# Kernel optimization log

Hardware: AMD Instinct MI355X
Metric: run time of the kernel (lower is better)

The kernel has to match this reference:

```python
import jax, jax.numpy as jnp
import numpy as np

B, T, C = 2, 4096, 1024
H = 16            # n_head (== n_groups == n_kv_heads)
HD = C // H       # head_dim = 64
W = 256           # window_size
ROPE_BASE = 10000.0


def _rope(x):
    # x: (B, H, T, HD); rotate interleaved pairs with position along axis 2
    t = x.shape[2]
    inv_freq = 1.0 / (ROPE_BASE ** (jnp.arange(0, HD, 2, dtype=jnp.float32) / HD))  # (HD/2,)
    freqs = jnp.arange(t, dtype=jnp.float32)[:, None] * inv_freq[None, :]           # (T, HD/2)
    cos = jnp.cos(freqs)[None, None].astype(x.dtype)
    sin = jnp.sin(freqs)[None, None].astype(x.dtype)
    x1, x2 = x[..., 0::2], x[..., 1::2]
    o1 = x1 * cos - x2 * sin
    o2 = x1 * sin + x2 * cos
    return jnp.stack([o1, o2], axis=-1).reshape(x.shape)


def setup_inputs() -> dict:
    key = jax.random.key(0)
    ks = jax.random.split(key, 5)
    s = 1.0 / np.sqrt(C)
    return {
        "x": jax.random.normal(ks[0], (B, T, C), dtype=jnp.float32),
        "wq": jax.random.normal(ks[1], (C, C), dtype=jnp.float32) * s,
        "wk": jax.random.normal(ks[2], (C, C), dtype=jnp.float32) * s,
        "wv": jax.random.normal(ks[3], (C, C), dtype=jnp.float32) * s,
        "wo": jax.random.normal(ks[4], (C, C), dtype=jnp.float32) * s,
    }


def reference(x, wq, wk, wv, wo):
    # projections (Linear stores (out, in) -> x @ w.T)
    q = jnp.einsum('btc,oc->bto', x, wq).reshape(B, T, H, HD).transpose(0, 2, 1, 3)
    k = jnp.einsum('btc,oc->bto', x, wk).reshape(B, T, H, HD).transpose(0, 2, 1, 3)
    v = jnp.einsum('btc,oc->bto', x, wv).reshape(B, T, H, HD).transpose(0, 2, 1, 3)

    q = _rope(q)
    k = _rope(k)

    nW = T // W
    qw = q.reshape(B, H, nW, W, HD)
    kw = k.reshape(B, H, nW, W, HD)
    vw = v.reshape(B, H, nW, W, HD)

    scale = 1.0 / jnp.sqrt(jnp.asarray(HD, dtype=q.dtype))
    att = jnp.einsum('bhnqd,bhnkd->bhnqk', qw, kw) * scale   # per-window, no causal mask
    att = jax.nn.softmax(att, axis=-1)
    yw = jnp.einsum('bhnqk,bhnkd->bhnqd', att, vw)

    y = yw.reshape(B, H, T, HD).transpose(0, 2, 1, 3).reshape(B, T, C)
    return jnp.einsum('btc,oc->bto', y, wo)
```

## Files before the change

### kernel.cpp

```cpp
#include <hip/hip_runtime.h>
#include <math.h>

typedef float f32x4 __attribute__((ext_vector_type(4)));
typedef __bf16 bf16x8 __attribute__((ext_vector_type(8)));
typedef _Float16 f16x4 __attribute__((ext_vector_type(4)));
typedef unsigned short ushort_t;

#define MFMA16(a, b, c) __builtin_amdgcn_mfma_f32_16x16x32_bf16((a), (b), (c), 0, 0, 0)
#define MFMAPV(a, b, c) __builtin_amdgcn_mfma_f32_16x16x16f16((a), (b), (c), 0, 0, 0)

static __device__ __forceinline__ ushort_t f2bf(float f) {
  union { float f; unsigned u; } v; v.f = f;
  unsigned u = v.u;
  return (ushort_t)((u + 0x7FFFu + ((u >> 16) & 1u)) >> 16);
}
static __device__ __forceinline__ float bf2f(ushort_t h) {
  union { unsigned u; float f; } v; v.u = ((unsigned)h) << 16;
  return v.f;
}
static __device__ __forceinline__ void gl_lds16(const void* g, void* lds_uniform) {
  __builtin_amdgcn_global_load_lds(
      (const __attribute__((address_space(1))) unsigned int*)g,
      (__attribute__((address_space(3))) unsigned int*)lds_uniform, 16, 0, 0);
}

__global__ void prep(const float* __restrict__ x,
                     const float* __restrict__ wq, const float* __restrict__ wk,
                     const float* __restrict__ wv, const float* __restrict__ wo,
                     ushort_t* __restrict__ Xb, ushort_t* __restrict__ Wqb,
                     ushort_t* __restrict__ Wkb, ushort_t* __restrict__ Wvb,
                     ushort_t* __restrict__ Wob, float2* __restrict__ cs) {
  const int bid = blockIdx.x;
  if (bid < 512) {
    int idx = bid * 256 + threadIdx.x;
    int pos = idx >> 5, i = idx & 31;
    double inv = exp2(-(double)i * 0.41524101186092029);
    double th = (double)pos * inv;
    double s, c;
    sincos(th, &s, &c);
    cs[idx] = make_float2((float)c, (float)s);
  } else {
    const float* src;
    ushort_t* dst;
    int i;
    if (bid < 8704) {
      src = x; dst = Xb;
      i = (bid - 512) * 256 + threadIdx.x;
    } else {
      const int wi = (bid - 8704) >> 10;
      src = (wi == 0) ? wq : (wi == 1) ? wk : (wi == 2) ? wv : wo;
      dst = (wi == 0) ? Wqb : (wi == 1) ? Wkb : (wi == 2) ? Wvb : Wob;
      i = ((bid - 8704) & 1023) * 256 + threadIdx.x;
    }
    f32x4 v = ((const f32x4*)src)[i];
    ushort4 o;
    o.x = f2bf(v.x); o.y = f2bf(v.y); o.z = f2bf(v.z); o.w = f2bf(v.w);
    ((ushort4*)dst)[i] = o;
  }
}

template <int MODE>
__global__ __launch_bounds__(256) void gemm_nt(
    const ushort_t* __restrict__ A,
    const ushort_t* __restrict__ W0, const ushort_t* __restrict__ W1, const ushort_t* __restrict__ W2,
    void* __restrict__ C0, void* __restrict__ C1, void* __restrict__ C2,
    int K, int N) {
  __shared__ __align__(16) ushort_t As[128 * 64];
  __shared__ __align__(16) ushort_t Bs[128 * 64];
  const int z = blockIdx.z;
  const ushort_t* W = (z == 0) ? W0 : (z == 1 ? W1 : W2);
  void* Cv = (z == 0) ? C0 : (z == 1 ? C1 : C2);

  const int t = threadIdx.x;
  const int lane = t & 63;
  const int l15 = lane & 15;
  const int quad = lane >> 4;
  const int wave = t >> 6;
  const int wm = wave & 1, wn = wave >> 1;
  const int bm = blockIdx.x, bn = blockIdx.y;

  const int srow = t >> 3;
  const int schunk = (t & 7) ^ (srow & 7);
  const ushort_t* Ag = A + (size_t)(bm * 128 + srow) * K + schunk * 8;
  const ushort_t* Wg = W + (size_t)(bn * 128 + srow) * K + schunk * 8;
  char* AsB = (char*)As + (t & 192) * 16;
  char* BsB = (char*)Bs + (t & 192) * 16;
  const size_t rK = (size_t)32 * K;

  const f32x4 zero4 = {0.f, 0.f, 0.f, 0.f};
  f32x4 acc[4][4];
#pragma unroll
  for (int i = 0; i < 4; ++i)
#pragma unroll
    for (int j = 0; j < 4; ++j) acc[i][j] = zero4;

  for (int kt = 0; kt < K; kt += 64) {
#pragma unroll
    for (int p = 0; p < 4; ++p) {
      gl_lds16(Ag + p * rK + kt, AsB + p * 4096);
      gl_lds16(Wg + p * rK + kt, BsB + p * 4096);
    }
    __syncthreads();
#pragma unroll
    for (int ks = 0; ks < 2; ++ks) {
      bf16x8 af[4], bfr[4];
#pragma unroll
      for (int i = 0; i < 4; ++i) {
        const int r = wm * 64 + i * 16 + l15;
        af[i] = *(const bf16x8*)&As[r * 64 + (((ks * 4 + quad) ^ (r & 7)) * 8)];
      }
#pragma unroll
      for (int j = 0; j < 4; ++j) {
        const int r = wn * 64 + j * 16 + l15;
        bfr[j] = *(const bf16x8*)&Bs[r * 64 + (((ks * 4 + quad) ^ (r & 7)) * 8)];
      }
#pragma unroll
      for (int i = 0; i < 4; ++i)
#pragma unroll
        for (int j = 0; j < 4; ++j) acc[i][j] = MFMA16(af[i], bfr[j], acc[i][j]);
    }
    __syncthreads();
  }

  const int rbase = bm * 128 + wm * 64 + quad * 4;
  const int cbase = bn * 128 + wn * 64 + l15;
#pragma unroll
  for (int i = 0; i < 4; ++i)
#pragma unroll
    for (int j = 0; j < 4; ++j)
#pragma unroll
      for (int r = 0; r < 4; ++r) {
        size_t idx = (size_t)(rbase + i * 16 + r) * N + (cbase + j * 16);
        if (MODE == 0) {
          ((float*)Cv)[idx] = acc[i][j][r];
        } else if (z == 2) {
          union { _Float16 h; ushort_t u; } cv;
          cv.h = (_Float16)acc[i][j][r];
          ((ushort_t*)Cv)[idx] = cv.u;
        } else {
          ((ushort_t*)Cv)[idx] = f2bf(acc[i][j][r]);
        }
      }
}

static __device__ __forceinline__ uint4 rope_u4(uint4 raw, const float2* __restrict__ c4,
                                                float scale) {
  unsigned rw[4] = {raw.x, raw.y, raw.z, raw.w};
  ushort_t o[8];
#pragma unroll
  for (int m = 0; m < 4; ++m) {
    float x1 = bf2f((ushort_t)(rw[m] & 0xffffu));
    float x2 = bf2f((ushort_t)(rw[m] >> 16));
    float2 sc = c4[m];
    o[2 * m]     = f2bf((x1 * sc.x - x2 * sc.y) * scale);
    o[2 * m + 1] = f2bf((x1 * sc.y + x2 * sc.x) * scale);
  }
  uint4 w;
  w.x = (unsigned)o[0] | ((unsigned)o[1] << 16);
  w.y = (unsigned)o[2] | ((unsigned)o[3] << 16);
  w.z = (unsigned)o[4] | ((unsigned)o[5] << 16);
  w.w = (unsigned)o[6] | ((unsigned)o[7] << 16);
  return w;
}

__global__ void ropeqk(ushort_t* __restrict__ Qb, ushort_t* __restrict__ Kb,
                       const float2* __restrict__ cs) {
  const int idx0 = blockIdx.x * 256 + threadIdx.x;
#pragma unroll
  for (int g = 0; g < 2; ++g) {
    const int idx = idx0 + g * 524288;
    const int row = idx >> 7;
    const int col8 = (idx & 127) << 3;
    const float2* c4 = cs + (((size_t)(row & 4095)) << 5) + ((col8 & 63) >> 1);
    uint4 q = ((const uint4*)Qb)[idx];
    uint4 k = ((const uint4*)Kb)[idx];
    ((uint4*)Qb)[idx] = rope_u4(q, c4, 0.125f);
    ((uint4*)Kb)[idx] = rope_u4(k, c4, 1.0f);
  }
}

__global__ __launch_bounds__(256) void attn(
    const ushort_t* __restrict__ Qb, const ushort_t* __restrict__ Kb,
    const ushort_t* __restrict__ Vb, ushort_t* __restrict__ Yb) {
  __shared__ __align__(16) ushort_t smem[16896];
  ushort_t* Ks = smem;
  ushort_t* Vt = smem;

  const int t = threadIdx.x;
  const int lane = t & 63, wave = t >> 6;
  const int l15 = lane & 15, quad = lane >> 4;
  const int qq = blockIdx.x >> 9;
  const int s = blockIdx.x & 511;
  const int win = s & 15, h = (s >> 4) & 15, b = s >> 8;
  const int kBase = win * 256;
  const int qRow0 = kBase + qq * 64 + wave * 16;
  const size_t gbase = ((size_t)b * 4096) * 1024 + h * 64;

  const int sr = t >> 3;
  const int c0 = (t & 7) * 8;

  const int schunk = ((t & 7) ^ (sr & 7)) * 8;
  const ushort_t* Kg = Kb + gbase + (size_t)(kBase + sr) * 1024 + schunk;
  char* LdsB = (char*)smem + (t & 192) * 16;
#pragma unroll
  for (int p = 0; p < 8; ++p) gl_lds16(Kg + (size_t)p * 32 * 1024, LdsB + p * 4096);

  bf16x8 qf[2];
#pragma unroll
  for (int ks = 0; ks < 2; ++ks)
    qf[ks] = *(const bf16x8*)(Qb + gbase + (size_t)(qRow0 + l15) * 1024 + ks * 32 + quad * 8);

  __syncthreads();

  const f32x4 zero4 = {0.f, 0.f, 0.f, 0.f};
  f32x4 S[16];
#pragma unroll
  for (int j = 0; j < 16; ++j) S[j] = zero4;
#pragma unroll
  for (int ks = 0; ks < 2; ++ks)
#pragma unroll
    for (int j = 0; j < 16; ++j) {
      bf16x8 kf = *(const bf16x8*)&Ks[(j * 16 + l15) * 64 + ((ks * 4 + quad) ^ (l15 & 7)) * 8];
      S[j] = MFMA16(kf, qf[ks], S[j]);
    }

  float mx = S[0][0];
#pragma unroll
  for (int j = 0; j < 16; ++j)
#pragma unroll
    for (int e = 0; e < 4; ++e) mx = fmaxf(mx, S[j][e]);
  mx = fmaxf(mx, __shfl_xor(mx, 16));
  mx = fmaxf(mx, __shfl_xor(mx, 32));
  float sum = 0.f;
#pragma unroll
  for (int j = 0; j < 16; ++j)
#pragma unroll
    for (int e = 0; e < 4; ++e) {
      float e_ = __expf(S[j][e] - mx);
      S[j][e] = e_;
      sum += e_;
    }
  sum += __shfl_xor(sum, 16);
  sum += __shfl_xor(sum, 32);
  const float linv = 1.0f / sum;

  f16x4 pf[16];
#pragma unroll
  for (int j = 0; j < 16; ++j) pf[j] = __builtin_convertvector(S[j], f16x4);

  uint4 vraw[8];
#pragma unroll
  for (int p = 0; p < 8; ++p)
    vraw[p] = *(const uint4*)(Vb + gbase + (size_t)(kBase + p * 32 + sr) * 1024 + c0);

  __syncthreads();

#pragma unroll
  for (int p = 0; p < 8; ++p) {
    const int k = p * 32 + sr;
    ushort_t vv[8];
    vv[0] = vraw[p].x & 0xffffu; vv[1] = vraw[p].x >> 16;
    vv[2] = vraw[p].y & 0xffffu; vv[3] = vraw[p].y >> 16;
    vv[4] = vraw[p].z & 0xffffu; vv[5] = vraw[p].z >> 16;
    vv[6] = vraw[p].w & 0xffffu; vv[7] = vraw[p].w >> 16;
#pragma unroll
    for (int e = 0; e < 8; ++e) {
      const int ee = (e + (t & 7)) & 7;
      Vt[(c0 + ee) * 264 + k] = vv[ee];
    }
  }
  __syncthreads();

  f32x4 O[4];
#pragma unroll
  for (int jd = 0; jd < 4; ++jd) O[jd] = zero4;
#pragma unroll
  for (int j = 0; j < 16; ++j)
#pragma unroll
    for (int jd = 0; jd < 4; ++jd) {
      f16x4 vf = *(const f16x4*)&Vt[(jd * 16 + l15) * 264 + j * 16 + quad * 4];
      O[jd] = MFMAPV(vf, pf[j], O[jd]);
    }

  __syncthreads();

  ushort_t* tile = smem + wave * 1152;
#pragma unroll
  for (int jd = 0; jd < 4; ++jd)
#pragma unroll
    for (int r = 0; r < 4; ++r)
      tile[l15 * 72 + jd * 16 + quad * 4 + r] = f2bf(O[jd][r] * linv);
#pragma unroll
  for (int g = 0; g < 2; ++g) {
    uint4 w = *(const uint4*)&tile[l15 * 72 + quad * 16 + g * 8];
    *(uint4*)(Yb + gbase + (size_t)(qRow0 + l15) * 1024 + quad * 16 + g * 8) = w;
  }
}

extern "C" void kernel_launch(void* const* d_in, const int* in_sizes, int n_in,
                              void* d_out, int out_size, void* d_ws, size_t ws_size,
                              hipStream_t stream) {
  (void)in_sizes; (void)n_in; (void)out_size; (void)ws_size;
  const float* x  = (const float*)d_in[0];
  const float* wq = (const float*)d_in[1];
  const float* wk = (const float*)d_in[2];
  const float* wv = (const float*)d_in[3];
  const float* wo = (const float*)d_in[4];

  char* ws = (char*)d_ws;
  ushort_t* Xb  = (ushort_t*)(ws);
  ushort_t* Wqb = (ushort_t*)(ws + 16777216);
  ushort_t* Wkb = Wqb + 1048576;
  ushort_t* Wvb = Wkb + 1048576;
  ushort_t* Wob = Wvb + 1048576;
  ushort_t* Qb  = (ushort_t*)(ws + 25165824);
  ushort_t* Kb  = Qb + 8388608;
  ushort_t* Vb  = Kb + 8388608;
  ushort_t* Yb  = Vb + 8388608;
  float2*   cs  = (float2*)(ws + 92274688);

  prep<<<dim3(12800), dim3(256), 0, stream>>>(x, wq, wk, wv, wo,
                                              Xb, Wqb, Wkb, Wvb, Wob, cs);

  gemm_nt<1><<<dim3(64, 8, 3), dim3(256), 0, stream>>>(
      Xb, Wqb, Wkb, Wvb, (void*)Qb, (void*)Kb, (void*)Vb, 1024, 1024);

  ropeqk<<<dim3(2048), dim3(256), 0, stream>>>(Qb, Kb, cs);

  attn<<<dim3(2048), dim3(256), 0, stream>>>(Qb, Kb, Vb, Yb);

  gemm_nt<0><<<dim3(64, 8, 1), dim3(256), 0, stream>>>(
      Yb, Wob, Wob, Wob, d_out, d_out, d_out, 1024, 1024);
}
```

Before: 231.5 us.

## Fuse RoPE into attention kernel and drop separate rope pass

```diff
diff --git a/kernel.cpp b/kernel.cpp
--- a/kernel.cpp
+++ b/kernel.cpp
@@ -4,6 +4,7 @@
 typedef float f32x4 __attribute__((ext_vector_type(4)));
 typedef __bf16 bf16x8 __attribute__((ext_vector_type(8)));
 typedef _Float16 f16x4 __attribute__((ext_vector_type(4)));
+typedef unsigned short u16x8 __attribute__((ext_vector_type(8)));
 typedef unsigned short ushort_t;
 
 #define MFMA16(a, b, c) __builtin_amdgcn_mfma_f32_16x16x32_bf16((a), (b), (c), 0, 0, 0)
@@ -17,6 +18,11 @@
 static __device__ __forceinline__ float bf2f(ushort_t h) {
   union { unsigned u; float f; } v; v.u = ((unsigned)h) << 16;
   return v.f;
+}
+static __device__ __forceinline__ ushort_t f2h_bits(float f) {
+  union { _Float16 h; ushort_t u; } v;
+  v.h = (_Float16)f;
+  return v.u;
 }
 static __device__ __forceinline__ void gl_lds16(const void* g, void* lds_uniform) {
   __builtin_amdgcn_global_load_lds(
@@ -59,7 +65,7 @@
   }
 }
 
-template <int MODE>
+template <int OUTBF>
 __global__ __launch_bounds__(256) void gemm_nt(
     const ushort_t* __restrict__ A,
     const ushort_t* __restrict__ W0, const ushort_t* __restrict__ W1, const ushort_t* __restrict__ W2,
@@ -131,58 +137,40 @@
 #pragma unroll
       for (int r = 0; r < 4; ++r) {
         size_t idx = (size_t)(rbase + i * 16 + r) * N + (cbase + j * 16);
-        if (MODE == 0) {
+        if (OUTBF)
+          ((ushort_t*)Cv)[idx] = f2bf(acc[i][j][r]);
+        else
           ((float*)Cv)[idx] = acc[i][j][r];
-        } else if (z == 2) {
-          union { _Float16 h; ushort_t u; } cv;
-          cv.h = (_Float16)acc[i][j][r];
-          ((ushort_t*)Cv)[idx] = cv.u;
-        } else {
-          ((ushort_t*)Cv)[idx] = f2bf(acc[i][j][r]);
-        }
       }
 }
 
-static __device__ __forceinline__ uint4 rope_u4(uint4 raw, const float2* __restrict__ c4,
-                                                float scale) {
+static __device__ __forceinline__ void rope8(const ushort_t* __restrict__ g,
+                                             ushort_t* __restrict__ lds,
+                                             const float2* __restrict__ cs4) {
+  uint4 raw = *(const uint4*)g;
   unsigned rw[4] = {raw.x, raw.y, raw.z, raw.w};
   ushort_t o[8];
 #pragma unroll
   for (int m = 0; m < 4; ++m) {
     float x1 = bf2f((ushort_t)(rw[m] & 0xffffu));
     float x2 = bf2f((ushort_t)(rw[m] >> 16));
-    float2 sc = c4[m];
-    o[2 * m]     = f2bf((x1 * sc.x - x2 * sc.y) * scale);
-    o[2 * m + 1] = f2bf((x1 * sc.y + x2 * sc.x) * scale);
+    float2 sc = cs4[m];
+    o[2 * m]     = f2bf(x1 * sc.x - x2 * sc.y);
+    o[2 * m + 1] = f2bf(x1 * sc.y + x2 * sc.x);
   }
   uint4 w;
   w.x = (unsigned)o[0] | ((unsigned)o[1] << 16);
   w.y = (unsigned)o[2] | ((unsigned)o[3] << 16);
   w.z = (unsigned)o[4] | ((unsigned)o[5] << 16);
   w.w = (unsigned)o[6] | ((unsigned)o[7] << 16);
-  return w;
-}
-
-__global__ void ropeqk(ushort_t* __restrict__ Qb, ushort_t* __restrict__ Kb,
-                       const float2* __restrict__ cs) {
-  const int idx0 = blockIdx.x * 256 + threadIdx.x;
-#pragma unroll
-  for (int g = 0; g < 2; ++g) {
-    const int idx = idx0 + g * 524288;
-    const int row = idx >> 7;
-    const int col8 = (idx & 127) << 3;
-    const float2* c4 = cs + (((size_t)(row & 4095)) << 5) + ((col8 & 63) >> 1);
-    uint4 q = ((const uint4*)Qb)[idx];
-    uint4 k = ((const uint4*)Kb)[idx];
-    ((uint4*)Qb)[idx] = rope_u4(q, c4, 0.125f);
-    ((uint4*)Kb)[idx] = rope_u4(k, c4, 1.0f);
-  }
+  *(uint4*)lds = w;
 }
 
 __global__ __launch_bounds__(256) void attn(
     const ushort_t* __restrict__ Qb, const ushort_t* __restrict__ Kb,
-    const ushort_t* __restrict__ Vb, ushort_t* __restrict__ Yb) {
-  __shared__ __align__(16) ushort_t smem[16896];
+    const ushort_t* __restrict__ Vb, ushort_t* __restrict__ Yb,
+    const float2* __restrict__ cs) {
+  __shared__ __align__(16) ushort_t smem[18432];
   ushort_t* Ks = smem;
   ushort_t* Vt = smem;
 
@@ -199,16 +187,29 @@
   const int sr = t >> 3;
   const int c0 = (t & 7) * 8;
 
-  const int schunk = ((t & 7) ^ (sr & 7)) * 8;
-  const ushort_t* Kg = Kb + gbase + (size_t)(kBase + sr) * 1024 + schunk;
-  char* LdsB = (char*)smem + (t & 192) * 16;
-#pragma unroll
-  for (int p = 0; p < 8; ++p) gl_lds16(Kg + (size_t)p * 32 * 1024, LdsB + p * 4096);
+#pragma unroll
+  for (int p = 0; p < 8; ++p) {
+    int r = p * 32 + sr;
+    rope8(Kb + gbase + (size_t)(kBase + r) * 1024 + c0, Ks + r * 72 + c0,
+          cs + (kBase + r) * 32 + (c0 >> 1));
+  }
 
   bf16x8 qf[2];
 #pragma unroll
-  for (int ks = 0; ks < 2; ++ks)
-    qf[ks] = *(const bf16x8*)(Qb + gbase + (size_t)(qRow0 + l15) * 1024 + ks * 32 + quad * 8);
+  for (int ks = 0; ks < 2; ++ks) {
+    union { u16x8 u; bf16x8 b; } aq;
+    aq.u = *(const u16x8*)(Qb + gbase + (size_t)(qRow0 + l15) * 1024 + ks * 32 + quad * 8);
+    const float2* csq = cs + (size_t)((qRow0 + l15) & 4095) * 32 + ks * 16 + quad * 4;
+#pragma unroll
+    for (int m = 0; m < 4; ++m) {
+      float x1 = bf2f(aq.u[2 * m]);
+      float x2 = bf2f(aq.u[2 * m + 1]);
+      float2 sc = csq[m];
+      aq.u[2 * m]     = f2bf((x1 * sc.x - x2 * sc.y) * 0.125f);
+      aq.u[2 * m + 1] = f2bf((x1 * sc.y + x2 * sc.x) * 0.125f);
+    }
+    qf[ks] = aq.b;
+  }
 
   __syncthreads();
 
@@ -220,7 +221,7 @@
   for (int ks = 0; ks < 2; ++ks)
 #pragma unroll
     for (int j = 0; j < 16; ++j) {
-      bf16x8 kf = *(const bf16x8*)&Ks[(j * 16 + l15) * 64 + ((ks * 4 + quad) ^ (l15 & 7)) * 8];
+      bf16x8 kf = *(const bf16x8*)&Ks[(j * 16 + l15) * 72 + ks * 32 + quad * 8];
       S[j] = MFMA16(kf, qf[ks], S[j]);
     }
 
@@ -259,10 +260,14 @@
   for (int p = 0; p < 8; ++p) {
     const int k = p * 32 + sr;
     ushort_t vv[8];
-    vv[0] = vraw[p].x & 0xffffu; vv[1] = vraw[p].x >> 16;
-    vv[2] = vraw[p].y & 0xffffu; vv[3] = vraw[p].y >> 16;
-    vv[4] = vraw[p].z & 0xffffu; vv[5] = vraw[p].z >> 16;
-    vv[6] = vraw[p].w & 0xffffu; vv[7] = vraw[p].w >> 16;
+    vv[0] = f2h_bits(bf2f((ushort_t)(vraw[p].x & 0xffffu)));
+    vv[1] = f2h_bits(bf2f((ushort_t)(vraw[p].x >> 16)));
+    vv[2] = f2h_bits(bf2f((ushort_t)(vraw[p].y & 0xffffu)));
+    vv[3] = f2h_bits(bf2f((ushort_t)(vraw[p].y >> 16)));
+    vv[4] = f2h_bits(bf2f((ushort_t)(vraw[p].z & 0xffffu)));
+    vv[5] = f2h_bits(bf2f((ushort_t)(vraw[p].z >> 16)));
+    vv[6] = f2h_bits(bf2f((ushort_t)(vraw[p].w & 0xffffu)));
+    vv[7] = f2h_bits(bf2f((ushort_t)(vraw[p].w >> 16)));
 #pragma unroll
     for (int e = 0; e < 8; ++e) {
       const int ee = (e + (t & 7)) & 7;
@@ -325,9 +330,7 @@
   gemm_nt<1><<<dim3(64, 8, 3), dim3(256), 0, stream>>>(
       Xb, Wqb, Wkb, Wvb, (void*)Qb, (void*)Kb, (void*)Vb, 1024, 1024);
 
-  ropeqk<<<dim3(2048), dim3(256), 0, stream>>>(Qb, Kb, cs);
-
-  attn<<<dim3(2048), dim3(256), 0, stream>>>(Qb, Kb, Vb, Yb);
+  attn<<<dim3(2048), dim3(256), 0, stream>>>(Qb, Kb, Vb, Yb, cs);
 
   gemm_nt<0><<<dim3(64, 8, 1), dim3(256), 0, stream>>>(
       Yb, Wob, Wob, Wob, d_out, d_out, d_out, 1024, 1024);
```

Result: no change. 230.3 us (-0.5%).
